# Kernel optimization log

Hardware: AMD Instinct MI355X
Metric: run time of the kernel (lower is better)

## Reference

```python
import jax, jax.numpy as jnp
import numpy as np
import math

IN_F, OUT_F = 512, 512
N_HEADS, N_SPLITS = 32, 4
N = 1024
DELTA_SCALE = 0.1


def setup_inputs() -> dict:
    key = jax.random.key(0)
    k_x, k_h, k_s, k_w = jax.random.split(key, 4)
    stdv = 1.0 / math.sqrt(OUT_F)
    inputs = {
        "input": jax.random.normal(k_x, (N, IN_F), dtype=jnp.float32),
        "head_ix": jax.random.randint(k_h, (N,), 0, N_HEADS, dtype=jnp.int32),
        "split_ix": jax.random.randint(k_s, (N,), 0, N_SPLITS, dtype=jnp.int32),
        # learned parameters (EmbeddingTensor tables)
        "weight": jax.random.uniform(k_w, (N_HEADS, IN_F, OUT_F), dtype=jnp.float32,
                                     minval=-stdv, maxval=stdv),
        "delta_weight": jnp.zeros((N_HEADS * N_SPLITS, IN_F, OUT_F), dtype=jnp.float32),
        "bias": jnp.zeros((N_HEADS, OUT_F), dtype=jnp.float32),
    }
    return inputs


def reference(input, head_ix, split_ix, weight, delta_weight, bias):
    # per-sample weight: base[head] + 0.1 * delta[head * n_splits + split]
    w = weight[head_ix] + delta_weight[head_ix * N_SPLITS + split_ix] * DELTA_SCALE  # [N, in, out]
    # batched vector-matrix multiply + per-head bias
    return jnp.einsum('ab,abc->ac', input, w) + bias[head_ix]  # [N, out]
```

## Files before the change

kernel.cpp:

```cpp
#include <hip/hip_runtime.h>

#define N_SAMP   1024
#define IN_F     512
#define OUT_F    512
#define N_HEADS  32
#define N_SPLITS 4
#define N_GROUPS (N_HEADS * N_SPLITS)
#define DELTA_SCALE 0.1f


typedef float f32x4 __attribute__((ext_vector_type(4)));

__device__ __forceinline__ f32x4 nt_load4(const float* p) {
    return __builtin_nontemporal_load((const f32x4*)p);
}
__device__ __forceinline__ void nt_store4(float* p, f32x4 v) {
    __builtin_nontemporal_store(v, (f32x4*)p);
}

__global__ __launch_bounds__(256, 2) void lms_fused_nt_w4(
    const float* __restrict__ X, const int* __restrict__ head_ix,
    const int* __restrict__ split_ix, const float* __restrict__ W,
    const float* __restrict__ D, const float* __restrict__ bias,
    float* __restrict__ out)
{
    constexpr int J    = 12;
    constexpr int KQ   = 16;
    constexpr int KT   = IN_F / KQ;
    constexpr int NST  = KT / 4;

    __shared__ float buf[J * IN_F];
    __shared__ int   list[N_SAMP];
    __shared__ int   wsum[4];

    const int g    = blockIdx.y;
    const int h    = g >> 2;
    const int c0   = blockIdx.x * 64;
    const int tid  = threadIdx.x;
    const int c4   = tid & 15;
    const int kq   = tid >> 4;
    const int lane = tid & 63;
    const int wave = tid >> 6;

    int run = 0;
    for (int r = 0; r < N_SAMP / 256; ++r) {
        const int i   = r * 256 + tid;
        const int key = head_ix[i] * N_SPLITS + split_ix[i];
        const bool hit = (key == g);
        const unsigned long long m = __ballot(hit);
        if (lane == 0) wsum[wave] = __popcll(m);
        __syncthreads();
        int base = run;
        for (int w = 0; w < 4; ++w)
            if (w < wave) base += wsum[w];
        if (hit)
            list[base + __popcll(m & ((1ULL << lane) - 1ULL))] = i;
        run += wsum[0] + wsum[1] + wsum[2] + wsum[3];
        __syncthreads();
    }
    const int total = run;
    if (total == 0) return;

    const size_t roff = (size_t)(kq * KT) * OUT_F + c0 + c4 * 4;
    const float* wp = W + (size_t)h * (IN_F * OUT_F) + roff;
    const float* dp = D + (size_t)g * (IN_F * OUT_F) + roff;

    for (int s0 = 0; s0 < total; s0 += J) {
        const int nc = min(total - s0, J);

        __syncthreads();
#pragma unroll
        for (int f = 0; f < 6; ++f) {
            const int i = f * 256 + tid;
            const int s = i >> 7, q = i & 127;
            float4 v = make_float4(0.f, 0.f, 0.f, 0.f);
            if (s < nc)
                v = *(const float4*)(X + (size_t)list[s0 + s] * IN_F + q * 4);
            *(float4*)(&buf[s * IN_F + q * 4]) = v;
        }
        __syncthreads();

        f32x4 acc[J];
#pragma unroll
        for (int j = 0; j < J; ++j) acc[j] = (f32x4)0.f;

        f32x4 rc[2][4];
        {
            f32x4 w0[4], d0[4];
#pragma unroll
            for (int u = 0; u < 4; ++u) {
                w0[u] = *(const f32x4*)(wp + (size_t)u * OUT_F);
                d0[u] = nt_load4(dp + (size_t)u * OUT_F);
            }
#pragma unroll
            for (int u = 0; u < 4; ++u)
                rc[0][u] = w0[u] + DELTA_SCALE * d0[u];
        }

#pragma unroll
        for (int st = 0; st < NST; ++st) {
            const int cb = st & 1, nb = cb ^ 1;
            const int nr = (st + 1 < NST) ? (st + 1) * 4 : st * 4;
            f32x4 wl[4], dl[4];
#pragma unroll
            for (int u = 0; u < 4; ++u) {
                wl[u] = *(const f32x4*)(wp + (size_t)(nr + u) * OUT_F);
                dl[u] = nt_load4(dp + (size_t)(nr + u) * OUT_F);
            }

            const float* xb = &buf[kq * KT + st * 4];
#pragma unroll
            for (int j = 0; j < J; ++j) {
                const float4 xv = *(const float4*)(xb + j * IN_F);
                acc[j] += xv.x * rc[cb][0];
                acc[j] += xv.y * rc[cb][1];
                acc[j] += xv.z * rc[cb][2];
                acc[j] += xv.w * rc[cb][3];
            }

#pragma unroll
            for (int u = 0; u < 4; ++u)
                rc[nb][u] = wl[u] + DELTA_SCALE * dl[u];
        }

        __syncthreads();
        f32x4* Red = (f32x4*)buf;
        if (kq < 8) {
#pragma unroll
            for (int j = 0; j < J; ++j)
                Red[(kq * J + j) * 16 + c4] = acc[j];
        }
        __syncthreads();
        if (kq >= 8) {
            const int q = kq - 8;
#pragma unroll
            for (int j = 0; j < J; ++j) {
                f32x4 r = Red[(q * J + j) * 16 + c4];
                Red[(q * J + j) * 16 + c4] = r + acc[j];
            }
        }
        __syncthreads();

        if (tid < J * 16) {
            const int j  = tid >> 4;
            const int cc = tid & 15;
            if (j < nc) {
                f32x4 s = (f32x4)0.f;
#pragma unroll
                for (int q = 0; q < 8; ++q)
                    s += Red[(q * J + j) * 16 + cc];
                const f32x4 bv = *(const f32x4*)(bias + (size_t)h * OUT_F
                                                 + c0 + cc * 4);
                float* op = out + (size_t)list[s0 + j] * OUT_F + c0 + cc * 4;
                nt_store4(op, s + bv);
            }
        }
    }
}

extern "C" void kernel_launch(void* const* d_in, const int* in_sizes, int n_in,
                              void* d_out, int out_size, void* d_ws, size_t ws_size,
                              hipStream_t stream) {
    const float* X        = (const float*)d_in[0];
    const int*   head_ix  = (const int*)d_in[1];
    const int*   split_ix = (const int*)d_in[2];
    const float* W        = (const float*)d_in[3];
    const float* D        = (const float*)d_in[4];
    const float* bias     = (const float*)d_in[5];
    float*       out      = (float*)d_out;

    dim3 gf(OUT_F / 64, N_GROUPS);
    lms_fused_nt_w4<<<gf, 256, 0, stream>>>(X, head_ix, split_ix, W, D, bias, out);
}
```

Baseline: 229.7 us.

## Split K dimension across blocks with workspace partials and separate reduce kernel

Instead of each block covering the full input dimension for a 64-column slice, blocks now cover 256 columns and a 128-row K chunk. Each block writes partial sums into a workspace laid out as 4 K-chunks, and a second kernel sums the partials and adds the bias. This changes the per-block work shape and the X staging footprint, while keeping the streaming weight-plus-delta reads. It adds a second launch and extra global traffic for partials (about 8 MB written and read back). The old fused kernel stays as a fallback when the workspace is too small.

Result: no change. 230.7 us (+0.4%).

```diff
diff --git a/kernel.cpp b/kernel.cpp
--- a/kernel.cpp
+++ b/kernel.cpp
@@ -16,6 +16,166 @@
 }
 __device__ __forceinline__ void nt_store4(float* p, f32x4 v) {
     __builtin_nontemporal_store(v, (f32x4*)p);
+}
+
+__global__ __launch_bounds__(256, 2) void lms_part1k(
+    const float* __restrict__ X, const int* __restrict__ head_ix,
+    const int* __restrict__ split_ix, const float* __restrict__ W,
+    const float* __restrict__ D, float* __restrict__ ws)
+{
+    constexpr int J    = 12;
+    constexpr int KRB  = 128;
+    constexpr int KRT  = 32;
+    constexpr int NST  = KRT / 4;
+
+    __shared__ float buf[2 * J * 64 * 4];
+    __shared__ int   list[N_SAMP];
+    __shared__ int   wsum[4];
+
+    const int g    = blockIdx.y;
+    const int h    = g >> 2;
+    const int ch   = blockIdx.x & 1;
+    const int kb   = blockIdx.x >> 1;
+    const int c0   = ch * 256;
+    const int tid  = threadIdx.x;
+    const int c4   = tid & 63;
+    const int kq   = tid >> 6;
+    const int lane = tid & 63;
+    const int wave = tid >> 6;
+
+    float (*Xs)[KRB] = (float(*)[KRB])buf;
+    f32x4* Red = (f32x4*)buf;
+
+    int run = 0;
+    for (int r = 0; r < N_SAMP / 256; ++r) {
+        const int i   = r * 256 + tid;
+        const int key = head_ix[i] * N_SPLITS + split_ix[i];
+        const bool hit = (key == g);
+        const unsigned long long m = __ballot(hit);
+        if (lane == 0) wsum[wave] = __popcll(m);
+        __syncthreads();
+        int base = run;
+        for (int w = 0; w < 4; ++w)
+            if (w < wave) base += wsum[w];
+        if (hit)
+            list[base + __popcll(m & ((1ULL << lane) - 1ULL))] = i;
+        run += wsum[0] + wsum[1] + wsum[2] + wsum[3];
+        __syncthreads();
+    }
+    const int total = run;
+    if (total == 0) return;
+
+    const int k0 = kb * KRB + kq * KRT;
+    const size_t roff = (size_t)k0 * OUT_F + c0 + 4 * c4;
+    const float* wp = W + (size_t)h * (IN_F * OUT_F) + roff;
+    const float* dp = D + (size_t)g * (IN_F * OUT_F) + roff;
+
+    for (int s0 = 0; s0 < total; s0 += J) {
+        const int nc = min(total - s0, J);
+
+        __syncthreads();
+        for (int f = 0; f < 2; ++f) {
+            const int i = f * 256 + tid;
+            if (i < J * (KRB / 4)) {
+                const int s = i >> 5, q = i & 31;
+                float4 v = make_float4(0.f, 0.f, 0.f, 0.f);
+                if (s < nc)
+                    v = *(const float4*)(X + (size_t)list[s0 + s] * IN_F
+                                         + kb * KRB + q * 4);
+                *(float4*)(&Xs[s][q * 4]) = v;
+            }
+        }
+        __syncthreads();
+
+        f32x4 acc[J];
+#pragma unroll
+        for (int j = 0; j < J; ++j) acc[j] = (f32x4)0.f;
+
+        f32x4 rc[2][4];
+        {
+            f32x4 w0[4], d0[4];
+#pragma unroll
+            for (int u = 0; u < 4; ++u) {
+                w0[u] = *(const f32x4*)(wp + (size_t)u * OUT_F);
+                d0[u] = nt_load4(dp + (size_t)u * OUT_F);
+            }
+#pragma unroll
+            for (int u = 0; u < 4; ++u)
+                rc[0][u] = w0[u] + DELTA_SCALE * d0[u];
+        }
+
+#pragma unroll 2
+        for (int st = 0; st < NST; ++st) {
+            const int cb = st & 1, nb = cb ^ 1;
+            const int nr = (st + 1 < NST) ? (st + 1) * 4 : st * 4;
+            f32x4 wl[4], dl[4];
+#pragma unroll
+            for (int u = 0; u < 4; ++u) {
+                wl[u] = *(const f32x4*)(wp + (size_t)(nr + u) * OUT_F);
+                dl[u] = nt_load4(dp + (size_t)(nr + u) * OUT_F);
+            }
+
+            const float* xb = &Xs[0][kq * KRT + st * 4];
+#pragma unroll
+            for (int j = 0; j < J; ++j) {
+                const float4 xv = *(const float4*)(xb + j * KRB);
+                acc[j] += xv.x * rc[cb][0];
+                acc[j] += xv.y * rc[cb][1];
+                acc[j] += xv.z * rc[cb][2];
+                acc[j] += xv.w * rc[cb][3];
+            }
+
+#pragma unroll
+            for (int u = 0; u < 4; ++u)
+                rc[nb][u] = wl[u] + DELTA_SCALE * dl[u];
+        }
+
+        __syncthreads();
+        if (kq < 2) {
+#pragma unroll
+            for (int j = 0; j < J; ++j)
+                Red[(kq * J + j) * 64 + c4] = acc[j];
+        }
+        __syncthreads();
+        if (kq >= 2) {
+            const int p = kq - 2;
+#pragma unroll
+            for (int j = 0; j < J; ++j) {
+                f32x4 r = Red[(p * J + j) * 64 + c4];
+                Red[(p * J + j) * 64 + c4] = r + acc[j];
+            }
+        }
+        __syncthreads();
+
+#pragma unroll
+        for (int t = 0; t < 3; ++t) {
+            const int oi = t * 256 + tid;
+            const int j  = oi >> 6, cc = oi & 63;
+            if (j < nc) {
+                const f32x4 s = Red[(0 * J + j) * 64 + cc]
+                              + Red[(1 * J + j) * 64 + cc];
+                float* op = ws + ((size_t)kb * N_SAMP + list[s0 + j]) * OUT_F
+                          + c0 + cc * 4;
+                nt_store4(op, s);
+            }
+        }
+    }
+}
+
+__global__ __launch_bounds__(256, 4) void lms_reduce4(
+    const float* __restrict__ ws, const int* __restrict__ head_ix,
+    const float* __restrict__ bias, float* __restrict__ out)
+{
+    const int gid = blockIdx.x * 256 + threadIdx.x;
+    const int i   = gid >> 7;
+    const int c4  = gid & 127;
+    const int h   = head_ix[i];
+
+    f32x4 s = *(const f32x4*)(bias + (size_t)h * OUT_F + 4 * c4);
+#pragma unroll
+    for (int p = 0; p < 4; ++p)
+        s += nt_load4(ws + ((size_t)p * N_SAMP + i) * OUT_F + 4 * c4);
+    *(f32x4*)(out + (size_t)i * OUT_F + 4 * c4) = s;
 }
 
 __global__ __launch_bounds__(256, 2) void lms_fused_nt_w4(
@@ -169,6 +329,16 @@
     const float* bias     = (const float*)d_in[5];
     float*       out      = (float*)d_out;
 
-    dim3 gf(OUT_F / 64, N_GROUPS);
-    lms_fused_nt_w4<<<gf, 256, 0, stream>>>(X, head_ix, split_ix, W, D, bias, out);
-}
+    const size_t ws_need = (size_t)4 * N_SAMP * OUT_F * sizeof(float);
+    if (ws_size >= ws_need) {
+        float* ws = (float*)d_ws;
+        lms_part1k<<<dim3(8, N_GROUPS), 256, 0, stream>>>(
+            X, head_ix, split_ix, W, D, ws);
+        lms_reduce4<<<dim3((N_SAMP * OUT_F / 4) / 256), 256, 0, stream>>>(
+            ws, head_ix, bias, out);
+    } else {
+        dim3 gf(OUT_F / 64, N_GROUPS);
+        lms_fused_nt_w4<<<gf, 256, 0, stream>>>(
+            X, head_ix, split_ix, W, D, bias, out);
+    }
+}
```
